# Optimization experiments

Measured on AMD Instinct MI355X. Metric: run time of the kernel, lower is better.

## Reference

```python
import jax, jax.numpy as jnp
import numpy as np

DIM = 1024
H = 16
D = DIM // H  # head_dim = 64
SCALE = 1.0 / np.sqrt(D)


def setup_inputs() -> dict:
    key = jax.random.key(0)
    ks = jax.random.split(key, 4)
    B, S = 4, 4096
    std = 1.0 / np.sqrt(DIM)
    return {
        "x": jax.random.normal(ks[0], (B, S, DIM), jnp.float32),
        "Wqkv": jax.random.normal(ks[1], (DIM, 3 * DIM), jnp.float32) * std,
        "bqkv": jnp.zeros((3 * DIM,), jnp.float32),
        "Wq": jax.random.normal(ks[2], (DIM, DIM), jnp.float32) * std,
        "bq": jnp.zeros((DIM,), jnp.float32),
        "Wproj": jax.random.normal(ks[3], (DIM, DIM), jnp.float32) * std,
        "bproj": jnp.zeros((DIM,), jnp.float32),
        "num_anchor_tokens": 512,
    }


def reference(x, Wqkv, bqkv, Wq, bq, Wproj, bproj, num_anchor_tokens):
    B, S, _ = x.shape
    A = num_anchor_tokens  # static Python int
    anchors = x[:, :A, :]          # (B, A, DIM)
    queries = x[:, A:, :]          # (B, Q, DIM)
    Q = S - A

    # Anchor tokens: full qkv projection
    qkv = anchors @ Wqkv + bqkv                      # (B, A, 3*DIM)
    qkv = qkv.reshape(B, A, 3, H, D)
    aq = jnp.transpose(qkv[:, :, 0], (0, 2, 1, 3))   # (B, H, A, D)
    ak = jnp.transpose(qkv[:, :, 1], (0, 2, 1, 3))   # (B, H, A, D)
    av = jnp.transpose(qkv[:, :, 2], (0, 2, 1, 3))   # (B, H, A, D)

    # Query tokens: query-only projection
    qq = (queries @ Wq + bq).reshape(B, Q, H, D)
    qq = jnp.transpose(qq, (0, 2, 1, 3))             # (B, H, Q, D)

    q_all = jnp.concatenate([aq, qq], axis=2)        # (B, H, S, D)

    # Everyone attends only to anchor keys/values
    scores = jnp.einsum("bhsd,bhad->bhsa", q_all, ak) * SCALE  # (B, H, S, A)
    attn = jax.nn.softmax(scores, axis=-1)
    out = jnp.einsum("bhsa,bhad->bhsd", attn, av)    # (B, H, S, D)
    out = jnp.transpose(out, (0, 2, 1, 3)).reshape(B, S, DIM)
    return out @ Wproj + bproj
```

## Files before the change

### kernel.cpp

```cpp
#include <hip/hip_runtime.h>
#include <hip/hip_bf16.h>

#define DIMC 1024
#define HC   16
#define DC   64
#define BC   4
#define SC   4096
#define ANC  512
#define QNC  3584
#define GK   1024
#define QSCALE (0.125f * 1.44269504088896f)

typedef __attribute__((ext_vector_type(4))) float f32x4;
typedef __attribute__((ext_vector_type(8))) short s16x8;
typedef __attribute__((ext_vector_type(4))) short s16x4;

__device__ inline short f2bf(float f) {
    unsigned u = __builtin_bit_cast(unsigned, f);
    u += 0x7fff + ((u >> 16) & 1);
    return (short)(u >> 16);
}
__device__ inline unsigned cvtpk(float lo, float hi) {
    unsigned d;
    asm("v_cvt_pk_bf16_f32 %0, %1, %2" : "=v"(d) : "v"(lo), "v"(hi));
    return d;
}

#define GLOAD16(gp, lp) __builtin_amdgcn_global_load_lds( \
    (const __attribute__((address_space(1))) void*)(gp),  \
    (__attribute__((address_space(3))) void*)(lp), 16, 0, 0)

__device__ __forceinline__ void tc_tile(
    const float* __restrict__ W, short* __restrict__ Wt, int K, int N,
    int bx, int by, float (*t)[33])
{
    const int tx = threadIdx.x & 31, ty = threadIdx.x >> 5;
    const int nt = bx * 32, kt = by * 32;
    #pragma unroll
    for (int j = 0; j < 4; ++j)
        t[ty + 8 * j][tx] = W[(size_t)(kt + ty + 8 * j) * N + nt + tx];
    __syncthreads();
    #pragma unroll
    for (int j = 0; j < 4; ++j)
        Wt[(size_t)(nt + ty + 8 * j) * K + kt + tx] = f2bf(t[tx][ty + 8 * j]);
}

__global__ __launch_bounds__(256) void prepass(
    const float* __restrict__ x, short* __restrict__ xb,
    const float* __restrict__ Wqkv, short* __restrict__ Wqkvt,
    const float* __restrict__ Wq, short* __restrict__ Wqt,
    const float* __restrict__ Wproj, short* __restrict__ Wprojt)
{
    __shared__ float t[32][33];
    const int b = blockIdx.x;
    if (b < 2048) {
        int i = b * 256 + threadIdx.x;
        for (; i < 4194304; i += 2048 * 256) {
            float4 v = ((const float4*)x)[i];
            s16x4 o = { f2bf(v.x), f2bf(v.y), f2bf(v.z), f2bf(v.w) };
            ((s16x4*)xb)[i] = o;
        }
    } else if (b < 5120) {
        const int z = b - 2048;
        tc_tile(Wqkv, Wqkvt, 1024, 3072, z % 96, z / 96, t);
    } else {
        const int z = b - 5120;
        const float* W = (z < 1024) ? Wq : Wproj;
        short* Wt = (z < 1024) ? Wqt : Wprojt;
        const int zz = z & 1023;
        tc_tile(W, Wt, 1024, 1024, zz & 31, zz >> 5, t);
    }
}

__device__ __forceinline__ void gemm_body(
    short* Als, short* Bls,
    const char* Arow0, const char* Brow0, const float* bias,
    float* outF, short* outQ, short* outK, short* outVt,
    int bm, int bn, int bb, int blocal, int rowOff, int mode)
{
    const int tid = threadIdx.x;
    const int wave = tid >> 6, lane = tid & 63;
    const int q = lane & 15, g = lane >> 4;
    const int wm = wave >> 1, wn = wave & 1;

    int srcOff[4], dstOff[4];
    #pragma unroll
    for (int p = 0; p < 4; ++p) {
        const int ca = p * 256 + tid;
        const int row = ca >> 3;
        const int cc = (ca & 7) ^ (row & 7);
        srcOff[p] = row * (GK * 2) + cc * 16;
        dstOff[p] = ca * 16;
    }

    f32x4 acc[4][4];
    #pragma unroll
    for (int i = 0; i < 4; ++i)
        #pragma unroll
        for (int j = 0; j < 4; ++j) acc[i][j] = (f32x4){0.f, 0.f, 0.f, 0.f};

    const int q7 = q & 7;

    for (int k0 = 0; k0 < GK; k0 += 64) {
        const int kb = k0 * 2;
        #pragma unroll
        for (int p = 0; p < 4; ++p)
            GLOAD16(Arow0 + srcOff[p] + kb, (char*)Als + dstOff[p]);
        #pragma unroll
        for (int p = 0; p < 4; ++p)
            GLOAD16(Brow0 + srcOff[p] + kb, (char*)Bls + dstOff[p]);
        __syncthreads();

        #pragma unroll
        for (int kk = 0; kk < 2; ++kk) {
            const int rc = ((kk * 4 + g) ^ q7) << 4;
            s16x8 aF[4], bF[4];
            #pragma unroll
            for (int mi = 0; mi < 4; ++mi)
                aF[mi] = *(const s16x8*)((const char*)Als +
                         (wm * 64 + mi * 16 + q) * 128 + rc);
            #pragma unroll
            for (int ni = 0; ni < 4; ++ni)
                bF[ni] = *(const s16x8*)((const char*)Bls +
                         (wn * 64 + ni * 16 + q) * 128 + rc);
            #pragma unroll
            for (int mi = 0; mi < 4; ++mi)
                #pragma unroll
                for (int ni = 0; ni < 4; ++ni)
                    acc[mi][ni] = __builtin_amdgcn_mfma_f32_16x16x32_bf16(
                        aF[mi], bF[ni], acc[mi][ni], 0, 0, 0);
        }
        __syncthreads();
    }

    #pragma unroll
    for (int ni = 0; ni < 4; ++ni) {
        const int col = bn + wn * 64 + ni * 16 + q;
        const float bv = bias[col];
        #pragma unroll
        for (int mi = 0; mi < 4; ++mi) {
            const int rl0 = blocal + wm * 64 + mi * 16 + 4 * g;
            #pragma unroll
            for (int r = 0; r < 4; ++r) {
                const int rl = rl0 + r;
                const float v = acc[mi][ni][r] + bv;
                if (mode == 2) {
                    outF[(size_t)(bm + wm * 64 + mi * 16 + 4 * g + r) * 1024 + col] = v;
                } else if (mode == 1) {
                    const int h = col >> 6, d = col & 63;
                    outQ[(((size_t)(bb * HC + h)) * SC + rowOff + rl) * DC + d] =
                        f2bf(v * QSCALE);
                } else {
                    const int which = col >> 10;
                    const int hd = col & 1023;
                    const int h = hd >> 6, d = hd & 63;
                    const size_t bh = (size_t)(bb * HC + h);
                    if (which == 0)
                        outQ[(bh * SC + rl) * DC + d] = f2bf(v * QSCALE);
                    else if (which == 1)
                        outK[(bh * ANC + rl) * DC + d] = f2bf(v);
                    else
                        outVt[(bh * DC + d) * ANC + rl] = f2bf(v);
                }
            }
        }
    }
}

__global__ __launch_bounds__(256) void gemm_k1k2(
    const short* __restrict__ xb,
    const short* __restrict__ Wqkvt, const float* __restrict__ bqkv,
    const short* __restrict__ Wqt,   const float* __restrict__ bq,
    short* __restrict__ Qb, short* __restrict__ Kb, short* __restrict__ Vtb)
{
    __shared__ __align__(16) short Als[128 * 64];
    __shared__ __align__(16) short Bls[128 * 64];

    const int i = blockIdx.x;
    const char* Arow0; const char* Brow0; const float* bias;
    int bm, bn, bb, blocal, rowOff, mode;
    if (i < 384) {
        const int c = i & 7, j = i >> 3;
        bn = (j % 24) * 128;
        bm = ((j / 24) * 8 + c) * 128;
        bb = bm / ANC; blocal = bm % ANC; rowOff = 0; mode = 0;
        Arow0 = (const char*)(xb + ((size_t)bb * SC + blocal) * GK);
        Brow0 = (const char*)(Wqkvt + (size_t)bn * GK);
        bias = bqkv;
    } else {
        const int i2 = i - 384;
        const int c = i2 & 7, j = i2 >> 3;
        bn = (j % 8) * 128;
        bm = ((j / 8) * 8 + c) * 128;
        bb = bm / QNC; blocal = bm % QNC; rowOff = ANC; mode = 1;
        Arow0 = (const char*)(xb + ((size_t)bb * SC + ANC + blocal) * GK);
        Brow0 = (const char*)(Wqt + (size_t)bn * GK);
        bias = bq;
    }
    gemm_body(Als, Bls, Arow0, Brow0, bias,
              nullptr, Qb, Kb, Vtb, bm, bn, bb, blocal, rowOff, mode);
}

__global__ __launch_bounds__(256) void gemm_proj(
    const short* __restrict__ Abase, const short* __restrict__ Bt,
    const float* __restrict__ bias, float* __restrict__ outF)
{
    __shared__ __align__(16) short Als[128 * 64];
    __shared__ __align__(16) short Bls[128 * 64];

    const int i = blockIdx.x;
    const int c = i & 7, j = i >> 3;
    const int bn = (j % 8) * 128;
    const int bm = ((j / 8) * 8 + c) * 128;
    const char* Arow0 = (const char*)(Abase + (size_t)bm * GK);
    const char* Brow0 = (const char*)(Bt + (size_t)bn * GK);
    gemm_body(Als, Bls, Arow0, Brow0, bias,
              outF, nullptr, nullptr, nullptr, bm, bn, 0, bm, 0, 2);
}

__global__ __launch_bounds__(512, 2) void attn_mfma(
    const short* __restrict__ Qb,
    const short* __restrict__ Kb,
    const short* __restrict__ Vtb,
    short* __restrict__ Aout)
{
    __shared__ __align__(16) char lds[147456];

    const int tid = threadIdx.x;
    const int wave = tid >> 6, lane = tid & 63;
    const int q = lane & 15, g = lane >> 4;
    const int q7 = q & 7;
    const int G = g ^ q7;
    const int bh = blockIdx.x >> 2;
    const int qc = blockIdx.x & 3;
    const int sbase = qc * 1024 + wave * 128;

    {
        const char* src = (const char*)(Kb + (size_t)bh * ANC * DC);
        #pragma unroll
        for (int l = 0; l < 8; ++l) {
            int i = l * 512 + tid;
            int row = i >> 3, cg = i & 7;
            union { float4 v; unsigned long long d[2]; } u;
            u.v = *(const float4*)(src + (size_t)i * 16);
            int kk = cg >> 2;
            int u0 = (2 * cg) & 7;
            int pc0 = 4 * kk + (u0 & 3);
            int hh = (u0 >> 2) << 3;
            int r7 = row & 7;
            char* dst = lds + row * 128;
            *(unsigned long long*)(dst + ((pc0 ^ r7) << 4) + hh) = u.d[0];
            *(unsigned long long*)(dst + (((pc0 + 1) ^ r7) << 4) + hh) = u.d[1];
        }
    }
    {
        const char* src = (const char*)(Vtb + (size_t)bh * DC * ANC);
        #pragma unroll
        for (int l = 0; l < 8; ++l) {
            int i = l * 512 + tid;
            int row = i >> 6, cg = i & 63;
            union { float4 v; unsigned long long d[2]; } u;
            u.v = *(const float4*)(src + (size_t)i * 16);
            int t2 = cg >> 2;
            int u0 = (2 * cg) & 7;
            int pc0 = 4 * t2 + (u0 & 3);
            int hh = (u0 >> 2) << 3;
            int r7 = row & 7;
            char* dst = lds + 65536 + row * 1024;
            *(unsigned long long*)(dst + ((pc0 ^ r7) << 4) + hh) = u.d[0];
            *(unsigned long long*)(dst + (((pc0 + 1) ^ r7) << 4) + hh) = u.d[1];
        }
    }
    __syncthreads();

    char* slot = lds + 131072 + wave * 2048;
    const int srow = lane >> 2, sc2 = lane & 3;
    const int sr7 = srow & 7;

    const int cgA = 2 * sc2, kkA = cgA >> 2, u0A = (2 * cgA) & 7;
    const int pcA = 4 * kkA + (u0A & 3), hA = (u0A >> 2) << 3;
    const int cgB = cgA + 1, kkB = cgB >> 2, u0B = (2 * cgB) & 7;
    const int pcB = 4 * kkB + (u0B & 3), hB = (u0B >> 2) << 3;
    const int wA0 = srow * 128 + ((pcA ^ sr7) << 4) + hA;
    const int wA1 = srow * 128 + (((pcA + 1) ^ sr7) << 4) + hA;
    const int wB0 = srow * 128 + ((pcB ^ sr7) << 4) + hB;
    const int wB1 = srow * 128 + (((pcB + 1) ^ sr7) << 4) + hB;
    const int wb0 = srow * 128 + (((sc2 * 2 + 0) ^ sr7) << 4);
    const int wb1 = srow * 128 + (((sc2 * 2 + 1) ^ sr7) << 4);
    const int sw = q7 << 4;

    const int off0 = G << 4, off1 = off0 ^ 64;
    const char* kb0 = lds + q * 128 + off0;
    const char* kb1 = lds + q * 128 + off1;
    const char* vregion = lds + 65536;
    const unsigned vo0 = (unsigned)((q +  0) * 1024 + off0);
    const unsigned vo1 = (unsigned)((q + 16) * 1024 + off0);
    const unsigned vo2 = (unsigned)((q + 32) * 1024 + off0);
    const unsigned vo3 = (unsigned)((q + 48) * 1024 + off0);

    const size_t qrow0 = (size_t)bh * SC;

    union { float4 v; unsigned long long d[2]; } gqA0, gqA1, gqB0, gqB1;
    {
        const char* QA = (const char*)(Qb + (qrow0 + sbase) * DC);
        gqA0.v = *(const float4*)(QA + lane * 32);
        gqA1.v = *(const float4*)(QA + lane * 32 + 16);
        const char* QB = QA + 16 * DC * 2;
        gqB0.v = *(const float4*)(QB + lane * 32);
        gqB1.v = *(const float4*)(QB + lane * 32 + 16);
    }

    for (int tp = 0; tp < 4; ++tp) {
        const int s0A = sbase + tp * 32;
        const int s0B = s0A + 16;

        *(unsigned long long*)(slot + wA0) = gqA0.d[0];
        *(unsigned long long*)(slot + wA1) = gqA0.d[1];
        *(unsigned long long*)(slot + wB0) = gqA1.d[0];
        *(unsigned long long*)(slot + wB1) = gqA1.d[1];
        __asm__ __volatile__("" ::: "memory");
        s16x8 qfA0 = *(const s16x8*)(slot + q * 128 + off0);
        s16x8 qfA1 = *(const s16x8*)(slot + q * 128 + off1);
        __asm__ __volatile__("" ::: "memory");
        *(unsigned long long*)(slot + wA0) = gqB0.d[0];
        *(unsigned long long*)(slot + wA1) = gqB0.d[1];
        *(unsigned long long*)(slot + wB0) = gqB1.d[0];
        *(unsigned long long*)(slot + wB1) = gqB1.d[1];
        __asm__ __volatile__("" ::: "memory");
        s16x8 qfB0 = *(const s16x8*)(slot + q * 128 + off0);
        s16x8 qfB1 = *(const s16x8*)(slot + q * 128 + off1);

        s16x8 pfA[16], pfB[16];
        float psA0 = 0.f, psA1 = 0.f, psA2 = 0.f, psA3 = 0.f;
        float psB0 = 0.f, psB1 = 0.f, psB2 = 0.f, psB3 = 0.f;
        __builtin_amdgcn_s_setprio(1);
        #pragma unroll
        for (int t2 = 0; t2 < 16; ++t2) {
            const int be = (2 * t2) * 2048, bo = be + 2048;
            s16x8 kfe0 = *(const s16x8*)(kb0 + be);
            s16x8 kfe1 = *(const s16x8*)(kb1 + be);
            f32x4 sA = (f32x4){0.f, 0.f, 0.f, 0.f};
            sA = __builtin_amdgcn_mfma_f32_16x16x32_bf16(kfe0, qfA0, sA, 0, 0, 0);
            sA = __builtin_amdgcn_mfma_f32_16x16x32_bf16(kfe1, qfA1, sA, 0, 0, 0);
            f32x4 sB = (f32x4){0.f, 0.f, 0.f, 0.f};
            sB = __builtin_amdgcn_mfma_f32_16x16x32_bf16(kfe0, qfB0, sB, 0, 0, 0);
            sB = __builtin_amdgcn_mfma_f32_16x16x32_bf16(kfe1, qfB1, sB, 0, 0, 0);
            s16x8 kfo0 = *(const s16x8*)(kb0 + bo);
            s16x8 kfo1 = *(const s16x8*)(kb1 + bo);
            f32x4 tA = (f32x4){0.f, 0.f, 0.f, 0.f};
            tA = __builtin_amdgcn_mfma_f32_16x16x32_bf16(kfo0, qfA0, tA, 0, 0, 0);
            tA = __builtin_amdgcn_mfma_f32_16x16x32_bf16(kfo1, qfA1, tA, 0, 0, 0);
            f32x4 tB = (f32x4){0.f, 0.f, 0.f, 0.f};
            tB = __builtin_amdgcn_mfma_f32_16x16x32_bf16(kfo0, qfB0, tB, 0, 0, 0);
            tB = __builtin_amdgcn_mfma_f32_16x16x32_bf16(kfo1, qfB1, tB, 0, 0, 0);

            float eA0 = exp2f(sA[0]), eA1 = exp2f(sA[1]);
            float eA2 = exp2f(sA[2]), eA3 = exp2f(sA[3]);
            float fA0 = exp2f(tA[0]), fA1 = exp2f(tA[1]);
            float fA2 = exp2f(tA[2]), fA3 = exp2f(tA[3]);
            psA0 += eA0 + fA0; psA1 += eA1 + fA1;
            psA2 += eA2 + fA2; psA3 += eA3 + fA3;
            float eB0 = exp2f(sB[0]), eB1 = exp2f(sB[1]);
            float eB2 = exp2f(sB[2]), eB3 = exp2f(sB[3]);
            float fB0 = exp2f(tB[0]), fB1 = exp2f(tB[1]);
            float fB2 = exp2f(tB[2]), fB3 = exp2f(tB[3]);
            psB0 += eB0 + fB0; psB1 += eB1 + fB1;
            psB2 += eB2 + fB2; psB3 += eB3 + fB3;

            union { s16x8 v; unsigned u[4]; } pkA, pkB;
            pkA.u[0] = cvtpk(eA0, eA1); pkA.u[1] = cvtpk(eA2, eA3);
            pkA.u[2] = cvtpk(fA0, fA1); pkA.u[3] = cvtpk(fA2, fA3);
            pfA[t2] = pkA.v;
            pkB.u[0] = cvtpk(eB0, eB1); pkB.u[1] = cvtpk(eB2, eB3);
            pkB.u[2] = cvtpk(fB0, fB1); pkB.u[3] = cvtpk(fB2, fB3);
            pfB[t2] = pkB.v;
        }
        __builtin_amdgcn_s_setprio(0);

        {
            const int snext = (tp < 3) ? (s0A + 32) : sbase;
            const char* QA = (const char*)(Qb + (qrow0 + snext) * DC);
            gqA0.v = *(const float4*)(QA + lane * 32);
            gqA1.v = *(const float4*)(QA + lane * 32 + 16);
            const char* QB = QA + 16 * DC * 2;
            gqB0.v = *(const float4*)(QB + lane * 32);
            gqB1.v = *(const float4*)(QB + lane * 32 + 16);
            __asm__ __volatile__("" :
                "+v"(gqA0.v.x), "+v"(gqA0.v.y), "+v"(gqA0.v.z), "+v"(gqA0.v.w),
                "+v"(gqA1.v.x), "+v"(gqA1.v.y), "+v"(gqA1.v.z), "+v"(gqA1.v.w),
                "+v"(gqB0.v.x), "+v"(gqB0.v.y), "+v"(gqB0.v.z), "+v"(gqB0.v.w),
                "+v"(gqB1.v.x), "+v"(gqB1.v.y), "+v"(gqB1.v.z), "+v"(gqB1.v.w));
        }

        float sumA = (psA0 + psA1) + (psA2 + psA3);
        sumA += __shfl_xor(sumA, 16);
        sumA += __shfl_xor(sumA, 32);
        const float rinvA = 1.0f / sumA;
        float sumB = (psB0 + psB1) + (psB2 + psB3);
        sumB += __shfl_xor(sumB, 16);
        sumB += __shfl_xor(sumB, 32);
        const float rinvB = 1.0f / sumB;

        f32x4 oaccA[4], oaccB[4];
        #pragma unroll
        for (int md = 0; md < 4; ++md) {
            oaccA[md] = (f32x4){0.f, 0.f, 0.f, 0.f};
            oaccB[md] = (f32x4){0.f, 0.f, 0.f, 0.f};
        }
        __builtin_amdgcn_s_setprio(1);
        #pragma unroll
        for (int t2 = 0; t2 < 16; ++t2) {
            const unsigned tx = (unsigned)(t2 << 6);
            s16x8 vf0 = *(const s16x8*)(vregion + (vo0 ^ tx));
            oaccA[0] = __builtin_amdgcn_mfma_f32_16x16x32_bf16(vf0, pfA[t2], oaccA[0], 0, 0, 0);
            oaccB[0] = __builtin_amdgcn_mfma_f32_16x16x32_bf16(vf0, pfB[t2], oaccB[0], 0, 0, 0);
            s16x8 vf1 = *(const s16x8*)(vregion + (vo1 ^ tx));
            oaccA[1] = __builtin_amdgcn_mfma_f32_16x16x32_bf16(vf1, pfA[t2], oaccA[1], 0, 0, 0);
            oaccB[1] = __builtin_amdgcn_mfma_f32_16x16x32_bf16(vf1, pfB[t2], oaccB[1], 0, 0, 0);
            s16x8 vf2 = *(const s16x8*)(vregion + (vo2 ^ tx));
            oaccA[2] = __builtin_amdgcn_mfma_f32_16x16x32_bf16(vf2, pfA[t2], oaccA[2], 0, 0, 0);
            oaccB[2] = __builtin_amdgcn_mfma_f32_16x16x32_bf16(vf2, pfB[t2], oaccB[2], 0, 0, 0);
            s16x8 vf3 = *(const s16x8*)(vregion + (vo3 ^ tx));
            oaccA[3] = __builtin_amdgcn_mfma_f32_16x16x32_bf16(vf3, pfA[t2], oaccA[3], 0, 0, 0);
            oaccB[3] = __builtin_amdgcn_mfma_f32_16x16x32_bf16(vf3, pfB[t2], oaccB[3], 0, 0, 0);
        }
        __builtin_amdgcn_s_setprio(0);

        __asm__ __volatile__("" ::: "memory");
        #pragma unroll
        for (int md = 0; md < 4; ++md) {
            union { unsigned long long d; unsigned u[2]; } ow;
            ow.u[0] = cvtpk(oaccA[md][0] * rinvA, oaccA[md][1] * rinvA);
            ow.u[1] = cvtpk(oaccA[md][2] * rinvA, oaccA[md][3] * rinvA);
            *(unsigned long long*)(slot + q * 128 + ((32 * md + 8 * g) ^ sw)) = ow.d;
        }
        __asm__ __volatile__("" ::: "memory");
        {
            float4 o0 = *(const float4*)(slot + wb0);
            float4 o1 = *(const float4*)(slot + wb1);
            char* Op = (char*)Aout +
                (((size_t)(bh >> 4) * SC + s0A + srow) * DIMC + (bh & 15) * DC) * 2 +
                sc2 * 32;
            *(float4*)(Op) = o0;
            *(float4*)(Op + 16) = o1;
        }
        __asm__ __volatile__("" ::: "memory");
        #pragma unroll
        for (int md = 0; md < 4; ++md) {
            union { unsigned long long d; unsigned u[2]; } ow;
            ow.u[0] = cvtpk(oaccB[md][0] * rinvB, oaccB[md][1] * rinvB);
            ow.u[1] = cvtpk(oaccB[md][2] * rinvB, oaccB[md][3] * rinvB);
            *(unsigned long long*)(slot + q * 128 + ((32 * md + 8 * g) ^ sw)) = ow.d;
        }
        __asm__ __volatile__("" ::: "memory");
        {
            float4 o0 = *(const float4*)(slot + wb0);
            float4 o1 = *(const float4*)(slot + wb1);
            char* Op = (char*)Aout +
                (((size_t)(bh >> 4) * SC + s0B + srow) * DIMC + (bh & 15) * DC) * 2 +
                sc2 * 32;
            *(float4*)(Op) = o0;
            *(float4*)(Op + 16) = o1;
        }
    }
}

extern "C" void kernel_launch(void* const* d_in, const int* in_sizes, int n_in,
                              void* d_out, int out_size, void* d_ws, size_t ws_size,
                              hipStream_t stream)
{
    (void)in_sizes; (void)n_in; (void)out_size; (void)ws_size;

    const float* x     = (const float*)d_in[0];
    const float* Wqkv  = (const float*)d_in[1];
    const float* bqkv  = (const float*)d_in[2];
    const float* Wq    = (const float*)d_in[3];
    const float* bq    = (const float*)d_in[4];
    const float* Wproj = (const float*)d_in[5];
    const float* bproj = (const float*)d_in[6];

    short* xb = (short*)d_out;
    short* Qb = xb + (size_t)16777216;
    short* Kb     = (short*)d_ws;
    short* Vtb    = Kb  + (size_t)2097152;
    short* Ab     = Vtb + (size_t)2097152;
    short* Wqkvt  = Ab  + (size_t)16777216;
    short* Wqt    = Wqkvt + (size_t)3145728;
    short* Wprojt = Wqt   + (size_t)1048576;

    prepass<<<dim3(7168), dim3(256), 0, stream>>>(
        x, xb, Wqkv, Wqkvt, Wq, Wqt, Wproj, Wprojt);

    gemm_k1k2<<<dim3(1280), dim3(256), 0, stream>>>(
        xb, Wqkvt, bqkv, Wqt, bq, Qb, Kb, Vtb);

    attn_mfma<<<dim3(256), dim3(512), 0, stream>>>(Qb, Kb, Vtb, Ab);

    gemm_proj<<<dim3(1024), dim3(256), 0, stream>>>(Ab, Wprojt, bproj, (float*)d_out);
}
```

Measured before the change: 190.0 us.

## Triple-buffer GEMM K-loop with async global-to-LDS prefetch and single barrier

Replaces the load-sync-compute-sync GEMM K-loop with a three-stage ring of 32-wide K tiles in LDS. Each phase waits on vmcnt and one barrier, issues the next stage's direct-to-LDS loads, then runs MFMAs on an earlier buffer, so global loads overlap compute. The swizzle is changed to fit 64-byte rows. LDS use per block rises from 32KB to 48KB, which can lower occupancy.

```diff
diff --git a/kernel.cpp b/kernel.cpp
--- a/kernel.cpp
+++ b/kernel.cpp
@@ -73,7 +73,7 @@
 }
 
 __device__ __forceinline__ void gemm_body(
-    short* Als, short* Bls,
+    char* AB,
     const char* Arow0, const char* Brow0, const float* bias,
     float* outF, short* outQ, short* outK, short* outVt,
     int bm, int bn, int bb, int blocal, int rowOff, int mode)
@@ -83,13 +83,13 @@
     const int q = lane & 15, g = lane >> 4;
     const int wm = wave >> 1, wn = wave & 1;
 
-    int srcOff[4], dstOff[4];
+    int srcOff[2], dstOff[2];
     #pragma unroll
-    for (int p = 0; p < 4; ++p) {
+    for (int p = 0; p < 2; ++p) {
         const int ca = p * 256 + tid;
-        const int row = ca >> 3;
-        const int cc = (ca & 7) ^ (row & 7);
-        srcOff[p] = row * (GK * 2) + cc * 16;
+        const int row = ca >> 2;
+        const int c = (ca & 3) ^ ((row >> 1) & 3);
+        srcOff[p] = row * (GK * 2) + c * 16;
         dstOff[p] = ca * 16;
     }
 
@@ -99,39 +99,62 @@
         #pragma unroll
         for (int j = 0; j < 4; ++j) acc[i][j] = (f32x4){0.f, 0.f, 0.f, 0.f};
 
-    const int q7 = q & 7;
-
-    for (int k0 = 0; k0 < GK; k0 += 64) {
-        const int kb = k0 * 2;
-        #pragma unroll
-        for (int p = 0; p < 4; ++p)
-            GLOAD16(Arow0 + srcOff[p] + kb, (char*)Als + dstOff[p]);
-        #pragma unroll
-        for (int p = 0; p < 4; ++p)
-            GLOAD16(Brow0 + srcOff[p] + kb, (char*)Bls + dstOff[p]);
-        __syncthreads();
-
-        #pragma unroll
-        for (int kk = 0; kk < 2; ++kk) {
-            const int rc = ((kk * 4 + g) ^ q7) << 4;
-            s16x8 aF[4], bF[4];
-            #pragma unroll
-            for (int mi = 0; mi < 4; ++mi)
-                aF[mi] = *(const s16x8*)((const char*)Als +
-                         (wm * 64 + mi * 16 + q) * 128 + rc);
-            #pragma unroll
-            for (int ni = 0; ni < 4; ++ni)
-                bF[ni] = *(const s16x8*)((const char*)Bls +
-                         (wn * 64 + ni * 16 + q) * 128 + rc);
-            #pragma unroll
-            for (int mi = 0; mi < 4; ++mi)
-                #pragma unroll
-                for (int ni = 0; ni < 4; ++ni)
-                    acc[mi][ni] = __builtin_amdgcn_mfma_f32_16x16x32_bf16(
-                        aF[mi], bF[ni], acc[mi][ni], 0, 0, 0);
-        }
-        __syncthreads();
-    }
+    const int rc = ((g ^ ((q >> 1) & 3)) << 4);
+
+#define STAGE(bufi, kt) do {                                            \
+        const int kb_ = (kt) * 64;       \
+        char* ab_ = AB + (bufi) * 8192;                                 \
+        char* bb_ = AB + 24576 + (bufi) * 8192;                         \
+        GLOAD16(Arow0 + srcOff[0] + kb_, ab_ + dstOff[0]);              \
+        GLOAD16(Arow0 + srcOff[1] + kb_, ab_ + dstOff[1]);              \
+        GLOAD16(Brow0 + srcOff[0] + kb_, bb_ + dstOff[0]);              \
+        GLOAD16(Brow0 + srcOff[1] + kb_, bb_ + dstOff[1]);              \
+    } while (0)
+
+#define COMPUTE(bufi) do {                                              \
+        const char* ab_ = AB + (bufi) * 8192;                           \
+        const char* bb_ = AB + 24576 + (bufi) * 8192;                   \
+        s16x8 aF[4], bF[4];                                             \
+        _Pragma("unroll")                                               \
+        for (int mi = 0; mi < 4; ++mi)                                  \
+            aF[mi] = *(const s16x8*)(ab_ + (wm * 64 + mi * 16 + q) * 64 + rc); \
+        _Pragma("unroll")                                               \
+        for (int ni = 0; ni < 4; ++ni)                                  \
+            bF[ni] = *(const s16x8*)(bb_ + (wn * 64 + ni * 16 + q) * 64 + rc); \
+        _Pragma("unroll")                                               \
+        for (int mi = 0; mi < 4; ++mi)                                  \
+            _Pragma("unroll")                                           \
+            for (int ni = 0; ni < 4; ++ni)                              \
+                acc[mi][ni] = __builtin_amdgcn_mfma_f32_16x16x32_bf16(  \
+                    aF[mi], bF[ni], acc[mi][ni], 0, 0, 0);              \
+    } while (0)
+
+#define PHASE4(stb, cb, kt) do {                                        \
+        asm volatile("s_waitcnt vmcnt(4)" ::: "memory");                \
+        __builtin_amdgcn_s_barrier();                                   \
+        STAGE(stb, kt);                                                 \
+        COMPUTE(cb);                                                    \
+    } while (0)
+
+    STAGE(0, 0);
+    STAGE(1, 1);
+
+    #pragma unroll 1
+    for (int t = 0; t < 30; t += 3) {
+        PHASE4(2, 0, t + 2);
+        PHASE4(0, 1, t + 3);
+        PHASE4(1, 2, t + 4);
+    }
+    asm volatile("s_waitcnt vmcnt(4)" ::: "memory");
+    __builtin_amdgcn_s_barrier();
+    COMPUTE(0);
+    asm volatile("s_waitcnt vmcnt(0)" ::: "memory");
+    __builtin_amdgcn_s_barrier();
+    COMPUTE(1);
+
+#undef PHASE4
+#undef STAGE
+#undef COMPUTE
 
     #pragma unroll
     for (int ni = 0; ni < 4; ++ni) {
@@ -173,8 +196,7 @@
     const short* __restrict__ Wqt,   const float* __restrict__ bq,
     short* __restrict__ Qb, short* __restrict__ Kb, short* __restrict__ Vtb)
 {
-    __shared__ __align__(16) short Als[128 * 64];
-    __shared__ __align__(16) short Bls[128 * 64];
+    __shared__ __align__(16) char AB[49152];
 
     const int i = blockIdx.x;
     const char* Arow0; const char* Brow0; const float* bias;
@@ -197,7 +219,7 @@
         Brow0 = (const char*)(Wqt + (size_t)bn * GK);
         bias = bq;
     }
-    gemm_body(Als, Bls, Arow0, Brow0, bias,
+    gemm_body(AB, Arow0, Brow0, bias,
               nullptr, Qb, Kb, Vtb, bm, bn, bb, blocal, rowOff, mode);
 }
 
@@ -205,8 +227,7 @@
     const short* __restrict__ Abase, const short* __restrict__ Bt,
     const float* __restrict__ bias, float* __restrict__ outF)
 {
-    __shared__ __align__(16) short Als[128 * 64];
-    __shared__ __align__(16) short Bls[128 * 64];
+    __shared__ __align__(16) char AB[49152];
 
     const int i = blockIdx.x;
     const int c = i & 7, j = i >> 3;
@@ -214,7 +235,7 @@
     const int bm = ((j / 8) * 8 + c) * 128;
     const char* Arow0 = (const char*)(Abase + (size_t)bm * GK);
     const char* Brow0 = (const char*)(Bt + (size_t)bn * GK);
-    gemm_body(Als, Bls, Arow0, Brow0, bias,
+    gemm_body(AB, Arow0, Brow0, bias,
               outF, nullptr, nullptr, nullptr, bm, bn, 0, bm, 0, 2);
 }
 
```

After: 178.2 us. 6.2% less time.
